# Kernel optimization log

Measured on AMD Instinct MI355X. Metric: run time of the kernel, lower is better.

Reference implementation:

```python
import jax, jax.numpy as jnp
import numpy as np

PRE_NMS = 256       # pre_nms_limit default
IOU_THRESH = 0.7    # iou_threshold default
POST_NMS = 128      # post_nms_limit default


def setup_inputs() -> dict:
    key = jax.random.key(0)
    ks = jax.random.split(key, 8)
    B, N, D = 16, 2048, 1024
    feats = jax.random.normal(ks[0], (B, N, D), dtype=jnp.float32)
    # valid boxes in (x1, y1, x2, y2) format
    xy1 = jax.random.uniform(ks[1], (B, N, 2), dtype=jnp.float32) * 1000.0
    wh = jax.random.uniform(ks[2], (B, N, 2), dtype=jnp.float32) * 200.0 + 1.0
    proposals = jnp.concatenate([xy1, xy1 + wh], axis=-1)
    def lin(k, fi, fo):
        return jax.random.normal(k, (fi, fo), dtype=jnp.float32) * (1.0 / np.sqrt(fi))
    Ws1 = lin(ks[3], D, 256); bs1 = jnp.zeros((256,), jnp.float32)
    Ws2 = lin(ks[4], 256, 64); bs2 = jnp.zeros((64,), jnp.float32)
    Wo1 = lin(ks[5], D, 256); bo1 = jnp.zeros((256,), jnp.float32)
    Wo2 = lin(ks[6], 256, 64); bo2 = jnp.zeros((64,), jnp.float32)
    return dict(feats=feats, proposals=proposals, Ws1=Ws1, bs1=bs1, Ws2=Ws2,
                bs2=bs2, Wo1=Wo1, bo1=bo1, Wo2=Wo2, bo2=bo2)


def _nms_keep(boxes, thresh):
    """Greedy NMS; boxes (P,4) already sorted by descending score."""
    P = boxes.shape[0]
    areas = (boxes[:, 2] - boxes[:, 0]) * (boxes[:, 3] - boxes[:, 1])
    lt = jnp.maximum(boxes[:, None, :2], boxes[None, :, :2])
    rb = jnp.minimum(boxes[:, None, 2:], boxes[None, :, 2:])
    wh = jnp.clip(rb - lt, 0.0)
    inter = wh[..., 0] * wh[..., 1]
    iou = inter / (areas[:, None] + areas[None, :] - inter)
    idx = jnp.arange(P)
    def body(i, keep):
        suppress = (iou[i] > thresh) & (idx > i) & keep[i]
        return keep & ~suppress
    return jax.lax.fori_loop(0, P, body, jnp.ones((P,), bool))


def _image_forward(f, boxes, Ws1, bs1, Ws2, bs2, Wo1, bo1, Wo2, bo2):
    # RelPNSimilarity: two small MLPs + sigmoid(subj @ obj^T)
    subj = jax.nn.relu(f @ Ws1 + bs1) @ Ws2 + bs2        # (N, 64)
    obj = jax.nn.relu(f @ Wo1 + bo1) @ Wo2 + bo2         # (N, 64)
    scores = jax.nn.sigmoid(subj @ obj.T)                # (N, N)
    N = f.shape[0]
    # full descending sort + take == top_k; flat index f = i*N + j -> pair (i, j)
    top_scores, top_idx = jax.lax.top_k(scores.reshape(-1), PRE_NMS)
    si = top_idx // N
    oi = top_idx % N
    pairs = jnp.stack([si, oi], axis=1)                  # (PRE_NMS, 2)
    b1 = boxes[si]
    b2 = boxes[oi]
    inter_boxes = jnp.concatenate(
        [jnp.maximum(b1[:, :2], b2[:, :2]), jnp.minimum(b1[:, 2:], b2[:, 2:])],
        axis=1)                                          # (PRE_NMS, 4)
    keep = _nms_keep(inter_boxes, IOU_THRESH)
    # kept indices in score order, padded with non-kept if fewer than POST_NMS
    P = PRE_NMS
    order = jnp.argsort(jnp.where(keep, jnp.arange(P), P + jnp.arange(P)))
    sel = order[:POST_NMS]
    valid = keep[sel]
    out_pairs = jnp.where(valid[:, None], pairs[sel], 0)
    out_scores = jnp.where(valid, top_scores[sel], 0.0)
    out_inter = jnp.where(valid[:, None], inter_boxes[sel], 0.0)
    return out_pairs, out_scores, out_inter, valid


def reference(feats, proposals, Ws1, bs1, Ws2, bs2, Wo1, bo1, Wo2, bo2):
    fn = jax.vmap(_image_forward,
                  in_axes=(0, 0, None, None, None, None, None, None, None, None))
    pairs, scores, inters, valid = fn(feats, proposals, Ws1, bs1, Ws2, bs2,
                                      Wo1, bo1, Wo2, bo2)
    # pairs (B,128,2) int, scores (B,128), inters (B,128,4), valid (B,128) bool
    return pairs, scores, inters, valid
```

## Files before the change

kernel.cpp:

```cpp
#include <hip/hip_runtime.h>
#include <stdint.h>


#define N_PROP 2048
#define D_FEAT 1024
#define H_DIM  256
#define E_DIM  64
#define BATCH  16
#define PRE_NMS 256
#define POST_NMS 128
#define CAND_CAP 32768
#define CNT_STRIDE 64
#define LOGIT_THRESH 11.0f
#define IOU_T 0.7f
#define WT_WHICH (16 * 32 * 512)
#define SO_ELEMS ((size_t)BATCH * 128 * 2 * 512)
#define LBUF_CAP 2048

typedef short sh8 __attribute__((ext_vector_type(8)));
typedef float f4  __attribute__((ext_vector_type(4)));

__device__ inline void decomp3(float f, unsigned& h, unsigned& m, unsigned& l) {
    unsigned u = __float_as_uint(f);
    h = (u + 0x8000u) & 0xFFFF0000u;
    float f1 = f - __uint_as_float(h);
    unsigned u1 = __float_as_uint(f1);
    m = (u1 + 0x8000u) & 0xFFFF0000u;
    float f2 = f1 - __uint_as_float(m);
    l = (__float_as_uint(f2) + 0x8000u) & 0xFFFF0000u;
}

__global__ __launch_bounds__(256) void prep_kernel(
    const float* __restrict__ Ws1, const float* __restrict__ Wo1,
    unsigned short* __restrict__ Wh, unsigned short* __restrict__ Wm,
    unsigned short* __restrict__ Wl)
{
    const int t = threadIdx.x;
    const int nblk = blockIdx.x;
    const int ks = blockIdx.y * 4 + (t >> 6);
    const int which = blockIdx.z;
    const float* W = which ? Wo1 : Ws1;
    const int lane = t & 63;
    const int q = lane >> 4, ln = lane & 15;

    unsigned hb[8], mb[8], lb[8];
#pragma unroll
    for (int j = 0; j < 8; ++j) {
        float v = W[(size_t)(ks * 32 + q * 8 + j) * H_DIM + nblk * 16 + ln];
        decomp3(v, hb[j], mb[j], lb[j]);
    }
    union { unsigned u[4]; sh8 v; } H, M, L;
#pragma unroll
    for (int c = 0; c < 4; ++c) {
        H.u[c] = (hb[2 * c] >> 16) | (hb[2 * c + 1] & 0xFFFF0000u);
        M.u[c] = (mb[2 * c] >> 16) | (mb[2 * c + 1] & 0xFFFF0000u);
        L.u[c] = (lb[2 * c] >> 16) | (lb[2 * c + 1] & 0xFFFF0000u);
    }
    size_t off = ((size_t)which * 16 * 32 + (size_t)nblk * 32 + ks) * 512 + lane * 8;
    *(sh8*)(Wh + off) = H.v;
    *(sh8*)(Wm + off) = M.v;
    *(sh8*)(Wl + off) = L.v;
}

__global__ __launch_bounds__(256) void mlp_kernel(
    const float* __restrict__ feats,
    const unsigned short* __restrict__ Wh, const unsigned short* __restrict__ Wm,
    const unsigned short* __restrict__ Wl,
    const float* __restrict__ bs1,
    const float* __restrict__ Ws2, const float* __restrict__ bs2,
    const float* __restrict__ bo1,
    const float* __restrict__ Wo2, const float* __restrict__ bo2,
    unsigned short* __restrict__ Sh, unsigned short* __restrict__ Sm,
    unsigned short* __restrict__ Sl,
    unsigned short* __restrict__ Oh, unsigned short* __restrict__ Om,
    unsigned short* __restrict__ Ol)
{
    const int t  = threadIdx.x;
    const int rt = blockIdx.x;
    const int b  = blockIdx.y;
    const int which = blockIdx.z;
    const float* B1 = which ? bo1 : bs1;
    const float* W2 = which ? Wo2 : Ws2;
    const float* B2 = which ? bo2 : bs2;
    unsigned short* Dh = which ? Oh : Sh;
    unsigned short* Dm = which ? Om : Sm;
    unsigned short* Dl = which ? Ol : Sl;
    const int r0g = rt * 64;

    const unsigned short* Whb = Wh + (size_t)which * WT_WHICH;
    const unsigned short* Wmb = Wm + (size_t)which * WT_WHICH;
    const unsigned short* Wlb = Wl + (size_t)which * WT_WHICH;

    __shared__ float lds[6208];
    float* Fs = lds;

    const int lane = t & 63;
    const int l15 = t & 15;
    const int q   = (t >> 4) & 3;
    const int wv  = t >> 6;
    const int wb  = wv * 64;

    f4 acc[4][4];
#pragma unroll
    for (int i = 0; i < 4; ++i)
#pragma unroll
        for (int j = 0; j < 4; ++j) acc[i][j] = (f4)0.0f;

    const float* fbase = feats + ((size_t)b * N_PROP + r0g) * D_FEAT;
    const int fm = t >> 2, fj = t & 3;

    float4 fpre0 = *(const float4*)(fbase + (size_t)fm * D_FEAT + 8 * fj);
    float4 fpre1 = *(const float4*)(fbase + (size_t)fm * D_FEAT + 8 * fj + 4);

    sh8 nxh, nxm, nxl;
    {
        size_t off = ((size_t)(wv * 4 + 0) * 32 + 0) * 512 + lane * 8;
        nxh = *(const sh8*)(Whb + off);
        nxm = *(const sh8*)(Wmb + off);
        nxl = *(const sh8*)(Wlb + off);
    }

    for (int kt = 0; kt < 32; ++kt) {
        __syncthreads();
        *(float4*)(Fs + fm * 36 + 8 * fj)     = fpre0;
        *(float4*)(Fs + fm * 36 + 8 * fj + 4) = fpre1;
        __syncthreads();
        if (kt + 1 < 32) {
            const int kn = (kt + 1) * 32;
            fpre0 = *(const float4*)(fbase + (size_t)fm * D_FEAT + kn + 8 * fj);
            fpre1 = *(const float4*)(fbase + (size_t)fm * D_FEAT + kn + 8 * fj + 4);
        }
        sh8 afh[4], afm[4], afl[4];
#pragma unroll
        for (int mt = 0; mt < 4; ++mt) {
            const float* src = Fs + (mt * 16 + l15) * 36 + q * 8;
            float4 a0 = *(const float4*)(src);
            float4 a1 = *(const float4*)(src + 4);
            float av[8] = {a0.x, a0.y, a0.z, a0.w, a1.x, a1.y, a1.z, a1.w};
            unsigned hb[8], mb[8], lb[8];
#pragma unroll
            for (int e = 0; e < 8; ++e) decomp3(av[e], hb[e], mb[e], lb[e]);
            union { unsigned u[4]; sh8 v; } H, M, L;
#pragma unroll
            for (int c = 0; c < 4; ++c) {
                H.u[c] = (hb[2 * c] >> 16) | (hb[2 * c + 1] & 0xFFFF0000u);
                M.u[c] = (mb[2 * c] >> 16) | (mb[2 * c + 1] & 0xFFFF0000u);
                L.u[c] = (lb[2 * c] >> 16) | (lb[2 * c + 1] & 0xFFFF0000u);
            }
            afh[mt] = H.v; afm[mt] = M.v; afl[mt] = L.v;
        }
#pragma unroll
        for (int nt = 0; nt < 4; ++nt) {
            sh8 cwh = nxh, cwm = nxm, cwl = nxl;
            int s = kt * 4 + nt + 1;
            if (s < 128) {
                int knt = s & 3, kkt = s >> 2;
                size_t off = ((size_t)(wv * 4 + knt) * 32 + kkt) * 512 + lane * 8;
                nxh = *(const sh8*)(Whb + off);
                nxm = *(const sh8*)(Wmb + off);
                nxl = *(const sh8*)(Wlb + off);
            }
#pragma unroll
            for (int mt = 0; mt < 4; ++mt) {
                f4 x = acc[mt][nt];
                x = __builtin_amdgcn_mfma_f32_16x16x32_bf16(afh[mt], cwh, x, 0, 0, 0);
                x = __builtin_amdgcn_mfma_f32_16x16x32_bf16(afh[mt], cwm, x, 0, 0, 0);
                x = __builtin_amdgcn_mfma_f32_16x16x32_bf16(afm[mt], cwh, x, 0, 0, 0);
                x = __builtin_amdgcn_mfma_f32_16x16x32_bf16(afh[mt], cwl, x, 0, 0, 0);
                x = __builtin_amdgcn_mfma_f32_16x16x32_bf16(afm[mt], cwm, x, 0, 0, 0);
                x = __builtin_amdgcn_mfma_f32_16x16x32_bf16(afl[mt], cwh, x, 0, 0, 0);
                acc[mt][nt] = x;
            }
        }
    }

    float bc[4];
#pragma unroll
    for (int nt = 0; nt < 4; ++nt) bc[nt] = B1[wb + nt * 16 + l15];

    float* Hp  = lds;
    float* W2c = lds + 4160;
    const int tr2 = t >> 4;
    const int tc2 = t & 15;
    float acc2[4][4];
#pragma unroll
    for (int i = 0; i < 4; ++i)
#pragma unroll
        for (int j = 0; j < 4; ++j) acc2[i][j] = 0.0f;

    float4 w2pre[2];
#pragma unroll
    for (int i = 0; i < 2; ++i) {
        int lin = (t + i * 256) * 4;
        int row = lin >> 6, col = lin & 63;
        w2pre[i] = *(const float4*)(W2 + (size_t)row * E_DIM + col);
    }

    for (int c = 0; c < 8; ++c) {
        const int p = c >> 1, ch = c & 1;
        __syncthreads();
        if (ch == 0 && wv == p) {
#pragma unroll
            for (int mt = 0; mt < 4; ++mt)
#pragma unroll
                for (int nt = 0; nt < 4; ++nt)
#pragma unroll
                    for (int r = 0; r < 4; ++r) {
                        float v = acc[mt][nt][r] + bc[nt];
                        v = v > 0.0f ? v : 0.0f;
                        Hp[(mt * 16 + q * 4 + r) * 65 + nt * 16 + l15] = v;
                    }
        }
#pragma unroll
        for (int i = 0; i < 2; ++i) {
            int lin = (t + i * 256) * 4;
            int row = lin >> 6, col = lin & 63;
            *(float4*)(W2c + row * 64 + col) = w2pre[i];
        }
        if (c + 1 < 8) {
            const int rbase = (c + 1) * 32;
#pragma unroll
            for (int i = 0; i < 2; ++i) {
                int lin = (t + i * 256) * 4;
                int row = lin >> 6, col = lin & 63;
                w2pre[i] = *(const float4*)(W2 + (size_t)(rbase + row) * E_DIM + col);
            }
        }
        __syncthreads();
#pragma unroll 8
        for (int kk = 0; kk < 32; ++kk) {
            int kl = ch * 32 + kk;
            float4 wvv = *(const float4*)(W2c + kk * 64 + tc2 * 4);
            float hv[4];
#pragma unroll
            for (int ri = 0; ri < 4; ++ri) hv[ri] = Hp[(tr2 * 4 + ri) * 65 + kl];
#pragma unroll
            for (int ri = 0; ri < 4; ++ri) {
                acc2[ri][0] = fmaf(hv[ri], wvv.x, acc2[ri][0]);
                acc2[ri][1] = fmaf(hv[ri], wvv.y, acc2[ri][1]);
                acc2[ri][2] = fmaf(hv[ri], wvv.z, acc2[ri][2]);
                acc2[ri][3] = fmaf(hv[ri], wvv.w, acc2[ri][3]);
            }
        }
    }

    {
        float bb[4] = {B2[tc2 * 4 + 0], B2[tc2 * 4 + 1],
                       B2[tc2 * 4 + 2], B2[tc2 * 4 + 3]};
        const int ks = tc2 >> 3, q2 = (tc2 >> 1) & 3, j0 = (tc2 & 1) * 4;
#pragma unroll
        for (int ri = 0; ri < 4; ++ri) {
            unsigned hb[4], mb[4], lb[4];
#pragma unroll
            for (int ci = 0; ci < 4; ++ci)
                decomp3(acc2[ri][ci] + bb[ci], hb[ci], mb[ci], lb[ci]);
            int row = r0g + tr2 * 4 + ri;
            int nblk = row >> 4, ln = row & 15;
            size_t so = (((size_t)b * 128 + nblk) * 2 + ks) * 512
                        + (q2 * 16 + ln) * 8 + j0;
            *(uint2*)(Dh + so) = make_uint2((hb[0] >> 16) | (hb[1] & 0xFFFF0000u),
                                            (hb[2] >> 16) | (hb[3] & 0xFFFF0000u));
            *(uint2*)(Dm + so) = make_uint2((mb[0] >> 16) | (mb[1] & 0xFFFF0000u),
                                            (mb[2] >> 16) | (mb[3] & 0xFFFF0000u));
            *(uint2*)(Dl + so) = make_uint2((lb[0] >> 16) | (lb[1] & 0xFFFF0000u),
                                            (lb[2] >> 16) | (lb[3] & 0xFFFF0000u));
        }
    }
}

__global__ __launch_bounds__(256) void score_kernel(
    const unsigned short* __restrict__ Sh, const unsigned short* __restrict__ Sm,
    const unsigned short* __restrict__ Sl,
    const unsigned short* __restrict__ Oh, const unsigned short* __restrict__ Om,
    const unsigned short* __restrict__ Ol,
    unsigned long long* __restrict__ cand, unsigned int* __restrict__ cnt)
{
    const int t = threadIdx.x;
    const int lane = t & 63;
    const int wv = t >> 6;
    const int rt = blockIdx.x >> 1;
    const int half = blockIdx.x & 1;
    const int b = blockIdx.y;
    const int r0g = rt * 64;
    const int ct0 = half * 16, ctEnd = ct0 + 16;
    const int l15 = t & 15;
    const int q   = (t >> 4) & 3;
    const int rh  = wv & 1;
    const int chh = wv >> 1;

    __shared__ unsigned long long lbuf[LBUF_CAP];
    __shared__ unsigned int lcnt, nOut, gbase;
    if (t == 0) lcnt = 0;
    __syncthreads();

    sh8 sfh[2][2], sfm[2][2], sfl[2][2];
#pragma unroll
    for (int mt = 0; mt < 2; ++mt)
#pragma unroll
        for (int ks = 0; ks < 2; ++ks) {
            size_t off = (((size_t)b * 128 + rt * 4 + rh * 2 + mt) * 2 + ks) * 512
                         + lane * 8;
            sfh[mt][ks] = *(const sh8*)(Sh + off);
            sfm[mt][ks] = *(const sh8*)(Sm + off);
            sfl[mt][ks] = *(const sh8*)(Sl + off);
        }

    sh8 oAh[2][2], oAm[2][2], oAl[2][2];
    sh8 oBh[2][2], oBm[2][2], oBl[2][2];

    auto load_o = [&](sh8 (&oh)[2][2], sh8 (&om)[2][2], sh8 (&ol)[2][2], int ct) {
        if (ct < ctEnd) {
#pragma unroll
            for (int nt = 0; nt < 2; ++nt)
#pragma unroll
                for (int ks = 0; ks < 2; ++ks) {
                    size_t off = (((size_t)b * 128 + ct * 4 + chh * 2 + nt) * 2 + ks) * 512
                                 + lane * 8;
                    oh[nt][ks] = *(const sh8*)(Oh + off);
                    om[nt][ks] = *(const sh8*)(Om + off);
                    ol[nt][ks] = *(const sh8*)(Ol + off);
                }
        }
    };

    auto compute = [&](sh8 (&oh)[2][2], sh8 (&om)[2][2], sh8 (&ol)[2][2], int ct) {
        f4 acc[2][2];
#pragma unroll
        for (int mt = 0; mt < 2; ++mt)
#pragma unroll
            for (int nt = 0; nt < 2; ++nt) {
                f4 x = (f4)0.0f;
#pragma unroll
                for (int ks = 0; ks < 2; ++ks) {
                    x = __builtin_amdgcn_mfma_f32_16x16x32_bf16(sfh[mt][ks], oh[nt][ks], x, 0, 0, 0);
                    x = __builtin_amdgcn_mfma_f32_16x16x32_bf16(sfh[mt][ks], om[nt][ks], x, 0, 0, 0);
                    x = __builtin_amdgcn_mfma_f32_16x16x32_bf16(sfm[mt][ks], oh[nt][ks], x, 0, 0, 0);
                    x = __builtin_amdgcn_mfma_f32_16x16x32_bf16(sfh[mt][ks], ol[nt][ks], x, 0, 0, 0);
                    x = __builtin_amdgcn_mfma_f32_16x16x32_bf16(sfm[mt][ks], om[nt][ks], x, 0, 0, 0);
                    x = __builtin_amdgcn_mfma_f32_16x16x32_bf16(sfl[mt][ks], oh[nt][ks], x, 0, 0, 0);
                }
                acc[mt][nt] = x;
            }
#pragma unroll
        for (int mt = 0; mt < 2; ++mt)
#pragma unroll
            for (int nt = 0; nt < 2; ++nt)
#pragma unroll
                for (int r = 0; r < 4; ++r) {
                    float logit = acc[mt][nt][r];
                    if (logit > LOGIT_THRESH) {
                        float score = 1.0f / (1.0f + expf(-logit));
                        unsigned sb = __float_as_uint(score);
                        int row = r0g + rh * 32 + mt * 16 + q * 4 + r;
                        int col = ct * 64 + chh * 32 + nt * 16 + l15;
                        unsigned flat = (unsigned)(row * N_PROP + col);
                        unsigned long long key =
                            ((unsigned long long)sb << 32) | (unsigned)(~flat);
                        unsigned p = atomicAdd(&lcnt, 1u);
                        if (p < LBUF_CAP) lbuf[p] = key;
                    }
                }
    };

    load_o(oAh, oAm, oAl, ct0);
    for (int i = 0; i < 16; i += 2) {
        load_o(oBh, oBm, oBl, ct0 + i + 1);
        compute(oAh, oAm, oAl, ct0 + i);
        load_o(oAh, oAm, oAl, ct0 + i + 2);
        compute(oBh, oBm, oBl, ct0 + i + 1);
    }

    __syncthreads();
    if (t == 0) {
        unsigned n = lcnt > LBUF_CAP ? LBUF_CAP : lcnt;
        nOut = n;
        gbase = n ? atomicAdd(&cnt[(size_t)b * CNT_STRIDE], n) : 0u;
    }
    __syncthreads();
    for (unsigned i = t; i < nOut; i += 256) {
        unsigned pos = gbase + i;
        if (pos < CAND_CAP) cand[(size_t)b * CAND_CAP + pos] = lbuf[i];
    }
}

__device__ inline void bitonic_sort_desc_u64(unsigned long long* a, unsigned n, int t) {
    for (unsigned k = 2; k <= n; k <<= 1)
        for (unsigned j = k >> 1; j > 0; j >>= 1) {
            __syncthreads();
            for (unsigned i = (unsigned)t; i < n; i += 256) {
                unsigned l = i ^ j;
                if (l > i) {
                    unsigned long long x = a[i], y = a[l];
                    bool up = ((i & k) == 0);
                    if (up ? (x < y) : (x > y)) { a[i] = y; a[l] = x; }
                }
            }
        }
    __syncthreads();
}

__global__ __launch_bounds__(256) void select_nms_kernel(
    const unsigned long long* __restrict__ cand, const unsigned int* __restrict__ cnt,
    const float* __restrict__ proposals, float* __restrict__ out)
{
    const int b = blockIdx.x;
    const int t = threadIdx.x;
    const int lane = t & 63;
    const int wv = t >> 6;
    __shared__ unsigned int hist[1024];
    __shared__ unsigned long long selk[256];
    __shared__ unsigned long long pool[4096];
    __shared__ unsigned int nDef, nPool, kc_s, need_s;
    __shared__ float bx1[256], by1[256], bx2[256], by2[256], barea[256];
    __shared__ unsigned int keepf[256];
    __shared__ unsigned int wcnt[4];

    unsigned count = cnt[(size_t)b * CNT_STRIDE];
    if (count > CAND_CAP) count = CAND_CAP;

    for (int i = t; i < 1024; i += 256) hist[i] = 0;
    selk[t] = 0ull;
    if (t == 0) { nDef = 0; nPool = 0; }
    __syncthreads();

    const unsigned long long* cb = cand + (size_t)b * CAND_CAP;
    for (unsigned i = t; i < count; i += 256) {
        unsigned k = 0x3F800000u - (unsigned)(cb[i] >> 32);
        if (k > 1023u) k = 1023u;
        atomicAdd(&hist[k], 1u);
    }
    __syncthreads();
    if (t == 0) {
        unsigned c = 0, kc = 1024, need = 0;
        for (int k = 0; k < 1024; ++k) {
            unsigned prev = c;
            c += hist[k];
            if (c >= PRE_NMS) { kc = (unsigned)k; need = PRE_NMS - prev; break; }
        }
        kc_s = kc; need_s = need;
    }
    __syncthreads();
    const unsigned kc = kc_s, need = need_s;

    for (unsigned i = t; i < count; i += 256) {
        unsigned long long key = cb[i];
        unsigned k = 0x3F800000u - (unsigned)(key >> 32);
        if (k > 1023u) k = 1023u;
        if (k < kc) {
            unsigned p = atomicAdd(&nDef, 1u);
            if (p < 256u) selk[p] = key;
        } else if (k == kc) {
            unsigned p = atomicAdd(&nPool, 1u);
            if (p < 4096u) pool[p] = key;
        }
    }
    __syncthreads();
    unsigned np = nPool; if (np > 4096u) np = 4096u;
    unsigned n2 = 256; while (n2 < np) n2 <<= 1;
    for (unsigned i = t; i < n2; i += 256) if (i >= np) pool[i] = 0ull;
    __syncthreads();
    bitonic_sort_desc_u64(pool, n2, t);

    unsigned nd = nDef; if (nd > 256u) nd = 256u;
    if ((unsigned)t < need && nd + (unsigned)t < 256u) selk[nd + t] = pool[t];
    __syncthreads();
    bitonic_sort_desc_u64(selk, 256u, t);

    float rx1, ry1, rx2, ry2, rar, rscore;
    int rsi, roi;
    {
        unsigned long long key = selk[t];
        unsigned flat = ~(unsigned)(key & 0xFFFFFFFFull);
        unsigned si = (flat >> 11) & 2047u;
        unsigned oi = flat & 2047u;
        rscore = __uint_as_float((unsigned)(key >> 32));
        const float* p1 = proposals + ((size_t)b * N_PROP + si) * 4;
        const float* p2 = proposals + ((size_t)b * N_PROP + oi) * 4;
        rx1 = fmaxf(p1[0], p2[0]);
        ry1 = fmaxf(p1[1], p2[1]);
        rx2 = fminf(p1[2], p2[2]);
        ry2 = fminf(p1[3], p2[3]);
        rar = (rx2 - rx1) * (ry2 - ry1);
        bx1[t] = rx1; by1[t] = ry1; bx2[t] = rx2; by2[t] = ry2; barea[t] = rar;
        rsi = (int)si; roi = (int)oi;
    }
    __syncthreads();

    bool kreg = true;
    for (int w = 0; w < 4; ++w) {
        if (wv == w) {
            for (int l = 0; l < 64; ++l) {
                int   ki  = __shfl((int)kreg, l);
                float ix1 = __shfl(rx1, l);
                float iy1 = __shfl(ry1, l);
                float ix2 = __shfl(rx2, l);
                float iy2 = __shfl(ry2, l);
                float iar = __shfl(rar, l);
                if (ki && lane > l) {
                    float lx = fmaxf(ix1, rx1), ly = fmaxf(iy1, ry1);
                    float rx = fminf(ix2, rx2), ry = fminf(iy2, ry2);
                    float wd = rx - lx; if (wd < 0.0f) wd = 0.0f;
                    float ht = ry - ly; if (ht < 0.0f) ht = 0.0f;
                    float inter = wd * ht;
                    float iou = inter / (iar + rar - inter);
                    if (iou > IOU_T) kreg = false;
                }
            }
            keepf[t] = kreg ? 1u : 0u;
        }
        __syncthreads();
        if (wv > w) {
            for (int l = 0; l < 64; ++l) {
                int i = w * 64 + l;
                if (keepf[i]) {
                    float lx = fmaxf(bx1[i], rx1), ly = fmaxf(by1[i], ry1);
                    float rx = fminf(bx2[i], rx2), ry = fminf(by2[i], ry2);
                    float wd = rx - lx; if (wd < 0.0f) wd = 0.0f;
                    float ht = ry - ly; if (ht < 0.0f) ht = 0.0f;
                    float inter = wd * ht;
                    float iou = inter / (barea[i] + rar - inter);
                    if (iou > IOU_T) kreg = false;
                }
            }
        }
    }
    __syncthreads();

    unsigned long long m = __ballot(kreg);
    unsigned before = __popcll(m & ((1ull << lane) - 1ull));
    if (lane == 0) wcnt[wv] = (unsigned)__popcll(m);
    __syncthreads();
    unsigned base = 0, tot = 0;
#pragma unroll
    for (int w = 0; w < 4; ++w) {
        unsigned c = wcnt[w];
        if (w < wv) base += c;
        tot += c;
    }
    unsigned kb = base + before;
    unsigned pos = kreg ? kb : (tot + (unsigned)t - kb);
    if (pos < POST_NMS) {
        bool valid = kreg;
        float* pairs = out;
        float* scr = out + (size_t)BATCH * POST_NMS * 2;
        float* itb = scr + (size_t)BATCH * POST_NMS;
        float* vld = itb + (size_t)BATCH * POST_NMS * 4;
        size_t s = (size_t)b * POST_NMS + pos;
        pairs[s * 2 + 0] = valid ? (float)rsi : 0.0f;
        pairs[s * 2 + 1] = valid ? (float)roi : 0.0f;
        scr[s] = valid ? rscore : 0.0f;
        itb[s * 4 + 0] = valid ? rx1 : 0.0f;
        itb[s * 4 + 1] = valid ? ry1 : 0.0f;
        itb[s * 4 + 2] = valid ? rx2 : 0.0f;
        itb[s * 4 + 3] = valid ? ry2 : 0.0f;
        vld[s] = valid ? 1.0f : 0.0f;
    }
}

extern "C" void kernel_launch(void* const* d_in, const int* in_sizes, int n_in,
                              void* d_out, int out_size, void* d_ws, size_t ws_size,
                              hipStream_t stream) {
    const float* feats     = (const float*)d_in[0];
    const float* proposals = (const float*)d_in[1];
    const float* Ws1 = (const float*)d_in[2];
    const float* bs1 = (const float*)d_in[3];
    const float* Ws2 = (const float*)d_in[4];
    const float* bs2 = (const float*)d_in[5];
    const float* Wo1 = (const float*)d_in[6];
    const float* bo1 = (const float*)d_in[7];
    const float* Wo2 = (const float*)d_in[8];
    const float* bo2 = (const float*)d_in[9];
    float* out = (float*)d_out;

    char* ws = (char*)d_ws;
    unsigned long long* cand = (unsigned long long*)ws;
    unsigned int* cnt = (unsigned int*)(cand + (size_t)BATCH * CAND_CAP);
    unsigned short* Wth = (unsigned short*)(cnt + BATCH * CNT_STRIDE);
    unsigned short* Wtm = Wth + 2 * WT_WHICH;
    unsigned short* Wtl = Wtm + 2 * WT_WHICH;
    unsigned short* Sh = Wtl + 2 * WT_WHICH;
    unsigned short* Sm = Sh + SO_ELEMS;
    unsigned short* Sl = Sm + SO_ELEMS;
    unsigned short* Oh = Sl + SO_ELEMS;
    unsigned short* Om = Oh + SO_ELEMS;
    unsigned short* Ol = Om + SO_ELEMS;

    hipMemsetAsync(cnt, 0, BATCH * CNT_STRIDE * sizeof(unsigned int), stream);

    prep_kernel<<<dim3(16, 8, 2), 256, 0, stream>>>(Ws1, Wo1, Wth, Wtm, Wtl);
    mlp_kernel<<<dim3(32, BATCH, 2), 256, 0, stream>>>(
        feats, Wth, Wtm, Wtl, bs1, Ws2, bs2, bo1, Wo2, bo2,
        Sh, Sm, Sl, Oh, Om, Ol);
    score_kernel<<<dim3(64, BATCH), 256, 0, stream>>>(
        Sh, Sm, Sl, Oh, Om, Ol, cand, cnt);
    select_nms_kernel<<<BATCH, 256, 0, stream>>>(cand, cnt, proposals, out);
}
```

Baseline: 574.5 us.

## Pre-split features into MFMA-ready bf16 triplets and use register-fed MLP kernel

Adds a kernel that splits the fp32 features once into high, mid and low bf16 parts, stored in the MFMA fragment layout in workspace. A new MLP kernel then loads the A and W fragments straight from global memory into registers, prefetching the next weight fragment, so no per-tile conversion or LDS staging is needed for the first layer. The cost is an extra pass that writes about 3x bf16 copies of the 128MB feature tensor, which also adds memory traffic. The new path only runs when the workspace is large enough, otherwise it falls back to the old kernel.

Result: slower. 693.6 us (+20.7%).

```diff
diff --git a/kernel.cpp b/kernel.cpp
--- a/kernel.cpp
+++ b/kernel.cpp
@@ -15,6 +15,7 @@
 #define IOU_T 0.7f
 #define WT_WHICH (16 * 32 * 512)
 #define SO_ELEMS ((size_t)BATCH * 128 * 2 * 512)
+#define A_ELEMS ((size_t)BATCH * 128 * 32 * 512)
 #define LBUF_CAP 2048
 
 typedef short sh8 __attribute__((ext_vector_type(8)));
@@ -60,6 +61,39 @@
     *(sh8*)(Wh + off) = H.v;
     *(sh8*)(Wm + off) = M.v;
     *(sh8*)(Wl + off) = L.v;
+}
+
+__global__ __launch_bounds__(256) void prep_feats_kernel(
+    const float* __restrict__ feats,
+    unsigned short* __restrict__ Fh, unsigned short* __restrict__ Fm,
+    unsigned short* __restrict__ Fl)
+{
+    const int t = threadIdx.x;
+    const int nblk = blockIdx.x;
+    const int ks = blockIdx.y * 4 + (t >> 6);
+    const int b = blockIdx.z;
+    const int lane = t & 63;
+    const int q = lane >> 4, ln = lane & 15;
+
+    const float* src = feats + ((size_t)b * N_PROP + nblk * 16 + ln) * D_FEAT
+                       + ks * 32 + q * 8;
+    float4 v0 = *(const float4*)src;
+    float4 v1 = *(const float4*)(src + 4);
+    float av[8] = {v0.x, v0.y, v0.z, v0.w, v1.x, v1.y, v1.z, v1.w};
+    unsigned hb[8], mb[8], lb[8];
+#pragma unroll
+    for (int j = 0; j < 8; ++j) decomp3(av[j], hb[j], mb[j], lb[j]);
+    union { unsigned u[4]; sh8 v; } H, M, L;
+#pragma unroll
+    for (int c = 0; c < 4; ++c) {
+        H.u[c] = (hb[2 * c] >> 16) | (hb[2 * c + 1] & 0xFFFF0000u);
+        M.u[c] = (mb[2 * c] >> 16) | (mb[2 * c + 1] & 0xFFFF0000u);
+        L.u[c] = (lb[2 * c] >> 16) | (lb[2 * c + 1] & 0xFFFF0000u);
+    }
+    size_t off = (((size_t)b * 128 + nblk) * 32 + ks) * 512 + (size_t)lane * 8;
+    *(sh8*)(Fh + off) = H.v;
+    *(sh8*)(Fm + off) = M.v;
+    *(sh8*)(Fl + off) = L.v;
 }
 
 __global__ __launch_bounds__(256) void mlp_kernel(
@@ -268,6 +302,188 @@
     }
 }
 
+__global__ __launch_bounds__(256) void mlp2_kernel(
+    const unsigned short* __restrict__ Fh, const unsigned short* __restrict__ Fm,
+    const unsigned short* __restrict__ Fl,
+    const unsigned short* __restrict__ Wh, const unsigned short* __restrict__ Wm,
+    const unsigned short* __restrict__ Wl,
+    const float* __restrict__ bs1,
+    const float* __restrict__ Ws2, const float* __restrict__ bs2,
+    const float* __restrict__ bo1,
+    const float* __restrict__ Wo2, const float* __restrict__ bo2,
+    unsigned short* __restrict__ Sh, unsigned short* __restrict__ Sm,
+    unsigned short* __restrict__ Sl,
+    unsigned short* __restrict__ Oh, unsigned short* __restrict__ Om,
+    unsigned short* __restrict__ Ol)
+{
+    const int t  = threadIdx.x;
+    const int rt = blockIdx.x;
+    const int b  = blockIdx.y;
+    const int which = blockIdx.z;
+    const float* B1 = which ? bo1 : bs1;
+    const float* W2 = which ? Wo2 : Ws2;
+    const float* B2 = which ? bo2 : bs2;
+    unsigned short* Dh = which ? Oh : Sh;
+    unsigned short* Dm = which ? Om : Sm;
+    unsigned short* Dl = which ? Ol : Sl;
+    const int r0g = rt * 64;
+
+    const unsigned short* Whb = Wh + (size_t)which * WT_WHICH;
+    const unsigned short* Wmb = Wm + (size_t)which * WT_WHICH;
+    const unsigned short* Wlb = Wl + (size_t)which * WT_WHICH;
+
+    __shared__ float lds[6208];
+
+    const int lane = t & 63;
+    const int l15 = t & 15;
+    const int q   = (t >> 4) & 3;
+    const int wv  = t >> 6;
+    const int wb  = wv * 64;
+
+    f4 acc[4][4];
+#pragma unroll
+    for (int i = 0; i < 4; ++i)
+#pragma unroll
+        for (int j = 0; j < 4; ++j) acc[i][j] = (f4)0.0f;
+
+    const size_t aoff0 = (((size_t)b * 128 + rt * 4) * 32) * 512 + (size_t)lane * 8;
+
+    sh8 nxh, nxm, nxl;
+    {
+        size_t off = ((size_t)(wv * 4 + 0) * 32 + 0) * 512 + lane * 8;
+        nxh = *(const sh8*)(Whb + off);
+        nxm = *(const sh8*)(Wmb + off);
+        nxl = *(const sh8*)(Wlb + off);
+    }
+
+    for (int kt = 0; kt < 32; ++kt) {
+        sh8 afh[4], afm[4], afl[4];
+#pragma unroll
+        for (int mt = 0; mt < 4; ++mt) {
+            size_t o = aoff0 + (size_t)mt * 16384 + (size_t)kt * 512;
+            afh[mt] = *(const sh8*)(Fh + o);
+            afm[mt] = *(const sh8*)(Fm + o);
+            afl[mt] = *(const sh8*)(Fl + o);
+        }
+#pragma unroll
+        for (int nt = 0; nt < 4; ++nt) {
+            sh8 cwh = nxh, cwm = nxm, cwl = nxl;
+            int s = kt * 4 + nt + 1;
+            if (s < 128) {
+                int knt = s & 3, kkt = s >> 2;
+                size_t off = ((size_t)(wv * 4 + knt) * 32 + kkt) * 512 + lane * 8;
+                nxh = *(const sh8*)(Whb + off);
+                nxm = *(const sh8*)(Wmb + off);
+                nxl = *(const sh8*)(Wlb + off);
+            }
+#pragma unroll
+            for (int mt = 0; mt < 4; ++mt) {
+                f4 x = acc[mt][nt];
+                x = __builtin_amdgcn_mfma_f32_16x16x32_bf16(afh[mt], cwh, x, 0, 0, 0);
+                x = __builtin_amdgcn_mfma_f32_16x16x32_bf16(afh[mt], cwm, x, 0, 0, 0);
+                x = __builtin_amdgcn_mfma_f32_16x16x32_bf16(afm[mt], cwh, x, 0, 0, 0);
+                x = __builtin_amdgcn_mfma_f32_16x16x32_bf16(afh[mt], cwl, x, 0, 0, 0);
+                x = __builtin_amdgcn_mfma_f32_16x16x32_bf16(afm[mt], cwm, x, 0, 0, 0);
+                x = __builtin_amdgcn_mfma_f32_16x16x32_bf16(afl[mt], cwh, x, 0, 0, 0);
+                acc[mt][nt] = x;
+            }
+        }
+    }
+
+    float bc[4];
+#pragma unroll
+    for (int nt = 0; nt < 4; ++nt) bc[nt] = B1[wb + nt * 16 + l15];
+
+    float* Hp  = lds;
+    float* W2c = lds + 4160;
+    const int tr2 = t >> 4;
+    const int tc2 = t & 15;
+    float acc2[4][4];
+#pragma unroll
+    for (int i = 0; i < 4; ++i)
+#pragma unroll
+        for (int j = 0; j < 4; ++j) acc2[i][j] = 0.0f;
+
+    float4 w2pre[2];
+#pragma unroll
+    for (int i = 0; i < 2; ++i) {
+        int lin = (t + i * 256) * 4;
+        int row = lin >> 6, col = lin & 63;
+        w2pre[i] = *(const float4*)(W2 + (size_t)row * E_DIM + col);
+    }
+
+    for (int c = 0; c < 8; ++c) {
+        const int p = c >> 1, ch = c & 1;
+        __syncthreads();
+        if (ch == 0 && wv == p) {
+#pragma unroll
+            for (int mt = 0; mt < 4; ++mt)
+#pragma unroll
+                for (int nt = 0; nt < 4; ++nt)
+#pragma unroll
+                    for (int r = 0; r < 4; ++r) {
+                        float v = acc[mt][nt][r] + bc[nt];
+                        v = v > 0.0f ? v : 0.0f;
+                        Hp[(mt * 16 + q * 4 + r) * 65 + nt * 16 + l15] = v;
+                    }
+        }
+#pragma unroll
+        for (int i = 0; i < 2; ++i) {
+            int lin = (t + i * 256) * 4;
+            int row = lin >> 6, col = lin & 63;
+            *(float4*)(W2c + row * 64 + col) = w2pre[i];
+        }
+        if (c + 1 < 8) {
+            const int rbase = (c + 1) * 32;
+#pragma unroll
+            for (int i = 0; i < 2; ++i) {
+                int lin = (t + i * 256) * 4;
+                int row = lin >> 6, col = lin & 63;
+                w2pre[i] = *(const float4*)(W2 + (size_t)(rbase + row) * E_DIM + col);
+            }
+        }
+        __syncthreads();
+#pragma unroll 8
+        for (int kk = 0; kk < 32; ++kk) {
+            int kl = ch * 32 + kk;
+            float4 wvv = *(const float4*)(W2c + kk * 64 + tc2 * 4);
+            float hv[4];
+#pragma unroll
+            for (int ri = 0; ri < 4; ++ri) hv[ri] = Hp[(tr2 * 4 + ri) * 65 + kl];
+#pragma unroll
+            for (int ri = 0; ri < 4; ++ri) {
+                acc2[ri][0] = fmaf(hv[ri], wvv.x, acc2[ri][0]);
+                acc2[ri][1] = fmaf(hv[ri], wvv.y, acc2[ri][1]);
+                acc2[ri][2] = fmaf(hv[ri], wvv.z, acc2[ri][2]);
+                acc2[ri][3] = fmaf(hv[ri], wvv.w, acc2[ri][3]);
+            }
+        }
+    }
+
+    {
+        float bb[4] = {B2[tc2 * 4 + 0], B2[tc2 * 4 + 1],
+                       B2[tc2 * 4 + 2], B2[tc2 * 4 + 3]};
+        const int ks = tc2 >> 3, q2 = (tc2 >> 1) & 3, j0 = (tc2 & 1) * 4;
+#pragma unroll
+        for (int ri = 0; ri < 4; ++ri) {
+            unsigned hb[4], mb[4], lb[4];
+#pragma unroll
+            for (int ci = 0; ci < 4; ++ci)
+                decomp3(acc2[ri][ci] + bb[ci], hb[ci], mb[ci], lb[ci]);
+            int row = r0g + tr2 * 4 + ri;
+            int nblk = row >> 4, ln = row & 15;
+            size_t so = (((size_t)b * 128 + nblk) * 2 + ks) * 512
+                        + (q2 * 16 + ln) * 8 + j0;
+            *(uint2*)(Dh + so) = make_uint2((hb[0] >> 16) | (hb[1] & 0xFFFF0000u),
+                                            (hb[2] >> 16) | (hb[3] & 0xFFFF0000u));
+            *(uint2*)(Dm + so) = make_uint2((mb[0] >> 16) | (mb[1] & 0xFFFF0000u),
+                                            (mb[2] >> 16) | (mb[3] & 0xFFFF0000u));
+            *(uint2*)(Dl + so) = make_uint2((lb[0] >> 16) | (lb[1] & 0xFFFF0000u),
+                                            (lb[2] >> 16) | (lb[3] & 0xFFFF0000u));
+        }
+    }
+}
+
 __global__ __launch_bounds__(256) void score_kernel(
     const unsigned short* __restrict__ Sh, const unsigned short* __restrict__ Sm,
     const unsigned short* __restrict__ Sl,
@@ -584,13 +800,24 @@
     unsigned short* Oh = Sl + SO_ELEMS;
     unsigned short* Om = Oh + SO_ELEMS;
     unsigned short* Ol = Om + SO_ELEMS;
+    unsigned short* Fh = Ol + SO_ELEMS;
+    unsigned short* Fm = Fh + A_ELEMS;
+    unsigned short* Fl = Fm + A_ELEMS;
+    size_t needed = (size_t)((char*)(Fl + A_ELEMS) - ws);
 
     hipMemsetAsync(cnt, 0, BATCH * CNT_STRIDE * sizeof(unsigned int), stream);
 
     prep_kernel<<<dim3(16, 8, 2), 256, 0, stream>>>(Ws1, Wo1, Wth, Wtm, Wtl);
-    mlp_kernel<<<dim3(32, BATCH, 2), 256, 0, stream>>>(
-        feats, Wth, Wtm, Wtl, bs1, Ws2, bs2, bo1, Wo2, bo2,
-        Sh, Sm, Sl, Oh, Om, Ol);
+    if (ws_size >= needed) {
+        prep_feats_kernel<<<dim3(128, 8, BATCH), 256, 0, stream>>>(feats, Fh, Fm, Fl);
+        mlp2_kernel<<<dim3(32, BATCH, 2), 256, 0, stream>>>(
+            Fh, Fm, Fl, Wth, Wtm, Wtl, bs1, Ws2, bs2, bo1, Wo2, bo2,
+            Sh, Sm, Sl, Oh, Om, Ol);
+    } else {
+        mlp_kernel<<<dim3(32, BATCH, 2), 256, 0, stream>>>(
+            feats, Wth, Wtm, Wtl, bs1, Ws2, bs2, bo1, Wo2, bo2,
+            Sh, Sm, Sl, Oh, Om, Ol);
+    }
     score_kernel<<<dim3(64, BATCH), 256, 0, stream>>>(
         Sh, Sm, Sl, Oh, Om, Ol, cand, cnt);
     select_nms_kernel<<<BATCH, 256, 0, stream>>>(cand, cnt, proposals, out);
```

## Fuse subject and object MLPs into one kernel sharing feature tiles

Applied to the files above, without the earlier changes.

The MLP kernel now computes both the subject and object branches in one block, so each loaded and bf16-decomposed feature tile feeds both weight sets instead of being read twice from global memory. To hold both accumulators, the row tile shrinks from 64 to 32 rows and the grid becomes 64x16 blocks with no z split. Per-block register pressure and the weight-load volume per output row rise, and the second-layer epilogue runs twice in sequence.

After: 592.0 us. +3.0%, slower.

```diff
diff --git a/kernel.cpp b/kernel.cpp
--- a/kernel.cpp
+++ b/kernel.cpp
@@ -62,7 +62,7 @@
     *(sh8*)(Wl + off) = L.v;
 }
 
-__global__ __launch_bounds__(256) void mlp_kernel(
+__global__ __launch_bounds__(256) void mlp_fused_kernel(
     const float* __restrict__ feats,
     const unsigned short* __restrict__ Wh, const unsigned short* __restrict__ Wm,
     const unsigned short* __restrict__ Wl,
@@ -78,20 +78,9 @@
     const int t  = threadIdx.x;
     const int rt = blockIdx.x;
     const int b  = blockIdx.y;
-    const int which = blockIdx.z;
-    const float* B1 = which ? bo1 : bs1;
-    const float* W2 = which ? Wo2 : Ws2;
-    const float* B2 = which ? bo2 : bs2;
-    unsigned short* Dh = which ? Oh : Sh;
-    unsigned short* Dm = which ? Om : Sm;
-    unsigned short* Dl = which ? Ol : Sl;
-    const int r0g = rt * 64;
-
-    const unsigned short* Whb = Wh + (size_t)which * WT_WHICH;
-    const unsigned short* Wmb = Wm + (size_t)which * WT_WHICH;
-    const unsigned short* Wlb = Wl + (size_t)which * WT_WHICH;
-
-    __shared__ float lds[6208];
+    const int r0g = rt * 32;
+
+    __shared__ float lds[4128];
     float* Fs = lds;
 
     const int lane = t & 63;
@@ -100,39 +89,38 @@
     const int wv  = t >> 6;
     const int wb  = wv * 64;
 
-    f4 acc[4][4];
-#pragma unroll
-    for (int i = 0; i < 4; ++i)
-#pragma unroll
-        for (int j = 0; j < 4; ++j) acc[i][j] = (f4)0.0f;
+    f4 acc[2][2][4];
+#pragma unroll
+    for (int w = 0; w < 2; ++w)
+#pragma unroll
+        for (int i = 0; i < 2; ++i)
+#pragma unroll
+            for (int j = 0; j < 4; ++j) acc[w][i][j] = (f4)0.0f;
 
     const float* fbase = feats + ((size_t)b * N_PROP + r0g) * D_FEAT;
-    const int fm = t >> 2, fj = t & 3;
-
-    float4 fpre0 = *(const float4*)(fbase + (size_t)fm * D_FEAT + 8 * fj);
-    float4 fpre1 = *(const float4*)(fbase + (size_t)fm * D_FEAT + 8 * fj + 4);
-
-    sh8 nxh, nxm, nxl;
-    {
-        size_t off = ((size_t)(wv * 4 + 0) * 32 + 0) * 512 + lane * 8;
-        nxh = *(const sh8*)(Whb + off);
-        nxm = *(const sh8*)(Wmb + off);
-        nxl = *(const sh8*)(Wlb + off);
+    const int fm = t >> 3, fj = t & 7;
+
+    float4 fpre = *(const float4*)(fbase + (size_t)fm * D_FEAT + fj * 4);
+
+    sh8 nxh[2], nxm[2], nxl[2];
+#pragma unroll
+    for (int w = 0; w < 2; ++w) {
+        size_t off = (size_t)w * WT_WHICH + ((size_t)(wv * 4) * 32) * 512 + lane * 8;
+        nxh[w] = *(const sh8*)(Wh + off);
+        nxm[w] = *(const sh8*)(Wm + off);
+        nxl[w] = *(const sh8*)(Wl + off);
     }
 
     for (int kt = 0; kt < 32; ++kt) {
         __syncthreads();
-        *(float4*)(Fs + fm * 36 + 8 * fj)     = fpre0;
-        *(float4*)(Fs + fm * 36 + 8 * fj + 4) = fpre1;
+        *(float4*)(Fs + fm * 36 + fj * 4) = fpre;
         __syncthreads();
-        if (kt + 1 < 32) {
-            const int kn = (kt + 1) * 32;
-            fpre0 = *(const float4*)(fbase + (size_t)fm * D_FEAT + kn + 8 * fj);
-            fpre1 = *(const float4*)(fbase + (size_t)fm * D_FEAT + kn + 8 * fj + 4);
-        }
-        sh8 afh[4], afm[4], afl[4];
-#pragma unroll
-        for (int mt = 0; mt < 4; ++mt) {
+        if (kt + 1 < 32)
+            fpre = *(const float4*)(fbase + (size_t)fm * D_FEAT + (kt + 1) * 32 + fj * 4);
+
+        sh8 afh[2], afm[2], afl[2];
+#pragma unroll
+        for (int mt = 0; mt < 2; ++mt) {
             const float* src = Fs + (mt * 16 + l15) * 36 + q * 8;
             float4 a0 = *(const float4*)(src);
             float4 a1 = *(const float4*)(src + 4);
@@ -149,121 +137,146 @@
             }
             afh[mt] = H.v; afm[mt] = M.v; afl[mt] = L.v;
         }
+
 #pragma unroll
         for (int nt = 0; nt < 4; ++nt) {
-            sh8 cwh = nxh, cwm = nxm, cwl = nxl;
+            sh8 cwh[2], cwm[2], cwl[2];
+#pragma unroll
+            for (int w = 0; w < 2; ++w) {
+                cwh[w] = nxh[w]; cwm[w] = nxm[w]; cwl[w] = nxl[w];
+            }
             int s = kt * 4 + nt + 1;
             if (s < 128) {
                 int knt = s & 3, kkt = s >> 2;
-                size_t off = ((size_t)(wv * 4 + knt) * 32 + kkt) * 512 + lane * 8;
-                nxh = *(const sh8*)(Whb + off);
-                nxm = *(const sh8*)(Wmb + off);
-                nxl = *(const sh8*)(Wlb + off);
-            }
-#pragma unroll
-            for (int mt = 0; mt < 4; ++mt) {
-                f4 x = acc[mt][nt];
-                x = __builtin_amdgcn_mfma_f32_16x16x32_bf16(afh[mt], cwh, x, 0, 0, 0);
-                x = __builtin_amdgcn_mfma_f32_16x16x32_bf16(afh[mt], cwm, x, 0, 0, 0);
-                x = __builtin_amdgcn_mfma_f32_16x16x32_bf16(afm[mt], cwh, x, 0, 0, 0);
-                x = __builtin_amdgcn_mfma_f32_16x16x32_bf16(afh[mt], cwl, x, 0, 0, 0);
-                x = __builtin_amdgcn_mfma_f32_16x16x32_bf16(afm[mt], cwm, x, 0, 0, 0);
-                x = __builtin_amdgcn_mfma_f32_16x16x32_bf16(afl[mt], cwh, x, 0, 0, 0);
-                acc[mt][nt] = x;
-            }
-        }
-    }
-
-    float bc[4];
-#pragma unroll
-    for (int nt = 0; nt < 4; ++nt) bc[nt] = B1[wb + nt * 16 + l15];
+#pragma unroll
+                for (int w = 0; w < 2; ++w) {
+                    size_t off = (size_t)w * WT_WHICH
+                               + ((size_t)(wv * 4 + knt) * 32 + kkt) * 512 + lane * 8;
+                    nxh[w] = *(const sh8*)(Wh + off);
+                    nxm[w] = *(const sh8*)(Wm + off);
+                    nxl[w] = *(const sh8*)(Wl + off);
+                }
+            }
+#pragma unroll
+            for (int w = 0; w < 2; ++w)
+#pragma unroll
+                for (int mt = 0; mt < 2; ++mt) {
+                    f4 x = acc[w][mt][nt];
+                    x = __builtin_amdgcn_mfma_f32_16x16x32_bf16(afh[mt], cwh[w], x, 0, 0, 0);
+                    x = __builtin_amdgcn_mfma_f32_16x16x32_bf16(afh[mt], cwm[w], x, 0, 0, 0);
+                    x = __builtin_amdgcn_mfma_f32_16x16x32_bf16(afm[mt], cwh[w], x, 0, 0, 0);
+                    x = __builtin_amdgcn_mfma_f32_16x16x32_bf16(afh[mt], cwl[w], x, 0, 0, 0);
+                    x = __builtin_amdgcn_mfma_f32_16x16x32_bf16(afm[mt], cwm[w], x, 0, 0, 0);
+                    x = __builtin_amdgcn_mfma_f32_16x16x32_bf16(afl[mt], cwh[w], x, 0, 0, 0);
+                    acc[w][mt][nt] = x;
+                }
+        }
+    }
+
+    float bc[2][4];
+#pragma unroll
+    for (int w = 0; w < 2; ++w) {
+        const float* B1 = w ? bo1 : bs1;
+#pragma unroll
+        for (int nt = 0; nt < 4; ++nt) bc[w][nt] = B1[wb + nt * 16 + l15];
+    }
 
     float* Hp  = lds;
-    float* W2c = lds + 4160;
+    float* W2c = lds + 2080;
     const int tr2 = t >> 4;
     const int tc2 = t & 15;
-    float acc2[4][4];
-#pragma unroll
-    for (int i = 0; i < 4; ++i)
-#pragma unroll
-        for (int j = 0; j < 4; ++j) acc2[i][j] = 0.0f;
-
-    float4 w2pre[2];
-#pragma unroll
-    for (int i = 0; i < 2; ++i) {
-        int lin = (t + i * 256) * 4;
-        int row = lin >> 6, col = lin & 63;
-        w2pre[i] = *(const float4*)(W2 + (size_t)row * E_DIM + col);
-    }
-
-    for (int c = 0; c < 8; ++c) {
-        const int p = c >> 1, ch = c & 1;
-        __syncthreads();
-        if (ch == 0 && wv == p) {
-#pragma unroll
-            for (int mt = 0; mt < 4; ++mt)
-#pragma unroll
-                for (int nt = 0; nt < 4; ++nt)
-#pragma unroll
-                    for (int r = 0; r < 4; ++r) {
-                        float v = acc[mt][nt][r] + bc[nt];
-                        v = v > 0.0f ? v : 0.0f;
-                        Hp[(mt * 16 + q * 4 + r) * 65 + nt * 16 + l15] = v;
-                    }
-        }
+
+#pragma unroll
+    for (int w = 0; w < 2; ++w) {
+        const float* W2 = w ? Wo2 : Ws2;
+        const float* B2 = w ? bo2 : bs2;
+        unsigned short* Dh = w ? Oh : Sh;
+        unsigned short* Dm = w ? Om : Sm;
+        unsigned short* Dl = w ? Ol : Sl;
+
+        float acc2[2][4];
+#pragma unroll
+        for (int i = 0; i < 2; ++i)
+#pragma unroll
+            for (int j = 0; j < 4; ++j) acc2[i][j] = 0.0f;
+
+        float4 w2pre[2];
 #pragma unroll
         for (int i = 0; i < 2; ++i) {
             int lin = (t + i * 256) * 4;
             int row = lin >> 6, col = lin & 63;
-            *(float4*)(W2c + row * 64 + col) = w2pre[i];
-        }
-        if (c + 1 < 8) {
-            const int rbase = (c + 1) * 32;
+            w2pre[i] = *(const float4*)(W2 + (size_t)row * E_DIM + col);
+        }
+
+        for (int c = 0; c < 8; ++c) {
+            const int p = c >> 1, ch = c & 1;
+            __syncthreads();
+            if (ch == 0 && wv == p) {
+#pragma unroll
+                for (int mt = 0; mt < 2; ++mt)
+#pragma unroll
+                    for (int nt = 0; nt < 4; ++nt)
+#pragma unroll
+                        for (int r = 0; r < 4; ++r) {
+                            float v = acc[w][mt][nt][r] + bc[w][nt];
+                            v = v > 0.0f ? v : 0.0f;
+                            Hp[(mt * 16 + q * 4 + r) * 65 + nt * 16 + l15] = v;
+                        }
+            }
 #pragma unroll
             for (int i = 0; i < 2; ++i) {
                 int lin = (t + i * 256) * 4;
                 int row = lin >> 6, col = lin & 63;
-                w2pre[i] = *(const float4*)(W2 + (size_t)(rbase + row) * E_DIM + col);
-            }
-        }
-        __syncthreads();
+                *(float4*)(W2c + row * 64 + col) = w2pre[i];
+            }
+            if (c + 1 < 8) {
+                const int rbase = (c + 1) * 32;
+#pragma unroll
+                for (int i = 0; i < 2; ++i) {
+                    int lin = (t + i * 256) * 4;
+                    int row = lin >> 6, col = lin & 63;
+                    w2pre[i] = *(const float4*)(W2 + (size_t)(rbase + row) * E_DIM + col);
+                }
+            }
+            __syncthreads();
 #pragma unroll 8
-        for (int kk = 0; kk < 32; ++kk) {
-            int kl = ch * 32 + kk;
-            float4 wvv = *(const float4*)(W2c + kk * 64 + tc2 * 4);
-            float hv[4];
-#pragma unroll
-            for (int ri = 0; ri < 4; ++ri) hv[ri] = Hp[(tr2 * 4 + ri) * 65 + kl];
-#pragma unroll
-            for (int ri = 0; ri < 4; ++ri) {
-                acc2[ri][0] = fmaf(hv[ri], wvv.x, acc2[ri][0]);
-                acc2[ri][1] = fmaf(hv[ri], wvv.y, acc2[ri][1]);
-                acc2[ri][2] = fmaf(hv[ri], wvv.z, acc2[ri][2]);
-                acc2[ri][3] = fmaf(hv[ri], wvv.w, acc2[ri][3]);
-            }
-        }
-    }
-
-    {
-        float bb[4] = {B2[tc2 * 4 + 0], B2[tc2 * 4 + 1],
-                       B2[tc2 * 4 + 2], B2[tc2 * 4 + 3]};
-        const int ks = tc2 >> 3, q2 = (tc2 >> 1) & 3, j0 = (tc2 & 1) * 4;
-#pragma unroll
-        for (int ri = 0; ri < 4; ++ri) {
-            unsigned hb[4], mb[4], lb[4];
-#pragma unroll
-            for (int ci = 0; ci < 4; ++ci)
-                decomp3(acc2[ri][ci] + bb[ci], hb[ci], mb[ci], lb[ci]);
-            int row = r0g + tr2 * 4 + ri;
-            int nblk = row >> 4, ln = row & 15;
-            size_t so = (((size_t)b * 128 + nblk) * 2 + ks) * 512
-                        + (q2 * 16 + ln) * 8 + j0;
-            *(uint2*)(Dh + so) = make_uint2((hb[0] >> 16) | (hb[1] & 0xFFFF0000u),
-                                            (hb[2] >> 16) | (hb[3] & 0xFFFF0000u));
-            *(uint2*)(Dm + so) = make_uint2((mb[0] >> 16) | (mb[1] & 0xFFFF0000u),
-                                            (mb[2] >> 16) | (mb[3] & 0xFFFF0000u));
-            *(uint2*)(Dl + so) = make_uint2((lb[0] >> 16) | (lb[1] & 0xFFFF0000u),
-                                            (lb[2] >> 16) | (lb[3] & 0xFFFF0000u));
+            for (int kk = 0; kk < 32; ++kk) {
+                int kl = ch * 32 + kk;
+                float4 wvv = *(const float4*)(W2c + kk * 64 + tc2 * 4);
+                float hv[2];
+#pragma unroll
+                for (int ri = 0; ri < 2; ++ri) hv[ri] = Hp[(tr2 * 2 + ri) * 65 + kl];
+#pragma unroll
+                for (int ri = 0; ri < 2; ++ri) {
+                    acc2[ri][0] = fmaf(hv[ri], wvv.x, acc2[ri][0]);
+                    acc2[ri][1] = fmaf(hv[ri], wvv.y, acc2[ri][1]);
+                    acc2[ri][2] = fmaf(hv[ri], wvv.z, acc2[ri][2]);
+                    acc2[ri][3] = fmaf(hv[ri], wvv.w, acc2[ri][3]);
+                }
+            }
+        }
+
+        {
+            float bb[4] = {B2[tc2 * 4 + 0], B2[tc2 * 4 + 1],
+                           B2[tc2 * 4 + 2], B2[tc2 * 4 + 3]};
+            const int ks = tc2 >> 3, q2 = (tc2 >> 1) & 3, j0 = (tc2 & 1) * 4;
+#pragma unroll
+            for (int ri = 0; ri < 2; ++ri) {
+                unsigned hb[4], mb[4], lb[4];
+#pragma unroll
+                for (int ci = 0; ci < 4; ++ci)
+                    decomp3(acc2[ri][ci] + bb[ci], hb[ci], mb[ci], lb[ci]);
+                int row = r0g + tr2 * 2 + ri;
+                int nblk = row >> 4, ln = row & 15;
+                size_t so = (((size_t)b * 128 + nblk) * 2 + ks) * 512
+                            + (q2 * 16 + ln) * 8 + j0;
+                *(uint2*)(Dh + so) = make_uint2((hb[0] >> 16) | (hb[1] & 0xFFFF0000u),
+                                                (hb[2] >> 16) | (hb[3] & 0xFFFF0000u));
+                *(uint2*)(Dm + so) = make_uint2((mb[0] >> 16) | (mb[1] & 0xFFFF0000u),
+                                                (mb[2] >> 16) | (mb[3] & 0xFFFF0000u));
+                *(uint2*)(Dl + so) = make_uint2((lb[0] >> 16) | (lb[1] & 0xFFFF0000u),
+                                                (lb[2] >> 16) | (lb[3] & 0xFFFF0000u));
+            }
         }
     }
 }
@@ -588,7 +601,7 @@
     hipMemsetAsync(cnt, 0, BATCH * CNT_STRIDE * sizeof(unsigned int), stream);
 
     prep_kernel<<<dim3(16, 8, 2), 256, 0, stream>>>(Ws1, Wo1, Wth, Wtm, Wtl);
-    mlp_kernel<<<dim3(32, BATCH, 2), 256, 0, stream>>>(
+    mlp_fused_kernel<<<dim3(64, BATCH), 256, 0, stream>>>(
         feats, Wth, Wtm, Wtl, bs1, Ws2, bs2, bo1, Wo2, bo2,
         Sh, Sm, Sl, Oh, Om, Ol);
     score_kernel<<<dim3(64, BATCH), 256, 0, stream>>>(
```
